# Optimization experiments

Hardware: AMD Instinct MI355X
Metric: run time of the kernel (lower is better)

Reference implementation:

```python
import jax, jax.numpy as jnp
import numpy as np

B, N, F = 2, 512, 64
LN_EPS = 1e-6

def _ln(x, scale, bias):
    mu = jnp.mean(x, axis=-1, keepdims=True)
    var = jnp.mean(jnp.square(x - mu), axis=-1, keepdims=True)
    return (x - mu) * jax.lax.rsqrt(var + LN_EPS) * scale + bias

def setup_inputs() -> dict:
    key = jax.random.key(0)
    k = jax.random.split(key, 16)
    w = lambda kk, s: jax.random.normal(kk, s, jnp.float32) * 0.02
    return {
        'qs': jax.random.normal(k[0], (B, N, F), jnp.float32),
        'ks': jax.random.normal(k[1], (B, N, F), jnp.float32),
        'vs': jax.random.normal(k[2], (B, N, F), jnp.float32),
        'qs_s': jax.random.normal(k[3], (B, N, 2), jnp.float32),
        'ks_s': jax.random.normal(k[4], (B, N, 2), jnp.float32),
        'qs_t': jax.random.uniform(k[5], (B, N, 1), dtype=jnp.float32),
        'ks_t': jax.random.uniform(k[6], (B, N, 1), dtype=jnp.float32),
        'valid_lens': jax.random.randint(k[7], (B,), 1, N + 1),
        'Wv': w(k[8], (F, 64)), 'bv': jnp.zeros((64,), jnp.float32),
        'Wa1': w(k[9], (2 * F + 5, 256)), 'ba1': jnp.zeros((256,), jnp.float32),
        'Wa2': w(k[10], (256, 256)), 'ba2': jnp.zeros((256,), jnp.float32),
        'Wa3': w(k[11], (256, 1)), 'ba3': jnp.zeros((1,), jnp.float32),
        'Wg1': w(k[12], (64, 256)), 'bg1': jnp.zeros((256,), jnp.float32),
        'Wg2': w(k[13], (256, 64)), 'bg2': jnp.zeros((64,), jnp.float32),
        'ln1_s': jnp.ones((64,), jnp.float32), 'ln1_b': jnp.zeros((64,), jnp.float32),
        'ln2_s': jnp.ones((64,), jnp.float32), 'ln2_b': jnp.zeros((64,), jnp.float32),
    }

def reference(qs, ks, vs, qs_s, ks_s, qs_t, ks_t, valid_lens,
              Wv, bv, Wa1, ba1, Wa2, ba2, Wa3, ba3,
              Wg1, bg1, Wg2, bg2, ln1_s, ln1_b, ln2_s, ln2_b):
    Bb, Q, Ff = qs.shape
    K = ks.shape[1]
    # pairwise broadcast-concat features: (B, Q, K, 2F+5)
    qb = jnp.broadcast_to(qs[:, :, None, :], (Bb, Q, K, Ff))
    kb = jnp.broadcast_to(ks[:, None, :, :], (Bb, Q, K, Ff))
    s_diff = qs_s[:, :, None, :] - ks_s[:, None, :, :]            # (B,Q,K,2)
    s_dist = jnp.linalg.norm(s_diff, axis=-1, keepdims=True)      # (B,Q,K,1)
    t_diff = qs_t[:, :, None, :] - ks_t[:, None, :, :]            # (B,Q,K,1)
    m = jnp.concatenate([qb, kb, s_diff, s_dist, jnp.square(s_dist), t_diff], axis=-1)
    # validity mask over the node axis (Q == K node-set attention)
    v_mask = (jnp.arange(K)[None, :] < valid_lens[:, None])[..., None]  # (B,K,1)
    mask = jnp.logical_and(v_mask, t_diff[..., 0] > 0)                   # (B,Q,K)
    # per-pair MLP attention score
    h = jax.nn.gelu(m @ Wa1 + ba1)
    h = jax.nn.gelu(h @ Wa2 + ba2)
    attn = (h @ Wa3 + ba3)[..., 0]                                       # (B,Q,K)
    attn = jnp.where(mask, attn, 0.0)
    vproj = vs @ Wv + bv                                                 # (B,K,64)
    ctx = _ln(jnp.einsum('bqk,bkd->bqd', attn, vproj), ln1_s, ln1_b)     # (B,Q,64)
    gate = jax.nn.gelu(ctx @ Wg1 + bg1) @ Wg2 + bg2                      # (B,Q,64)
    pooled = jnp.max(jnp.where(v_mask, gate * ctx, -jnp.inf), axis=1)    # (B,64)
    vnode = _ln(pooled, ln2_s, ln2_b)
    return ctx, vnode
```

## Files before the change

kernel.cpp:

```cpp
#include <hip/hip_runtime.h>
#include <math.h>

#define BB 2
#define NN 512
#define FF 64
#define HH 256
#define LN_EPS 1e-6f

typedef __attribute__((ext_vector_type(8))) short short8v;
typedef __attribute__((ext_vector_type(4))) float float4v;

#define LDAH 264

#if __has_builtin(__builtin_amdgcn_exp2f)
#define EXP2F(x) __builtin_amdgcn_exp2f(x)
#else
#define EXP2F(x) exp2f(x)
#endif
#if __has_builtin(__builtin_amdgcn_sqrtf)
#define SQRTF(x) __builtin_amdgcn_sqrtf(x)
#else
#define SQRTF(x) sqrtf(x)
#endif

__device__ __forceinline__ float gelu_tanh(float x) {
    float x2 = x * x;
    float t  = __builtin_fmaf(0.10294340f, x2, 2.30211830f);
    float e  = EXP2F(x * t);
    float r  = __builtin_amdgcn_rcpf(e + 1.0f);
    return __builtin_fmaf(-x, r, x);
}

__device__ __forceinline__ unsigned short f2bf(float f) {
    unsigned u = __float_as_uint(f);
    unsigned r = u + 0x7fffu + ((u >> 16) & 1u);
    return (unsigned short)(r >> 16);
}

__device__ __forceinline__ unsigned enc_f(float f) {
    unsigned b = __float_as_uint(f);
    return (b & 0x80000000u) ? ~b : (b | 0x80000000u);
}
__device__ __forceinline__ float dec_f(unsigned u) {
    return __uint_as_float((u & 0x80000000u) ? (u ^ 0x80000000u) : ~u);
}

__global__ __launch_bounds__(256) void prep_kernel(
    const float* __restrict__ qs, const float* __restrict__ ks,
    const float* __restrict__ vs,
    const float* __restrict__ Wa1, const float* __restrict__ ba1,
    const float* __restrict__ Wv,  const float* __restrict__ bv,
    const float* __restrict__ Wa2,
    const float* __restrict__ qs_t, const float* __restrict__ ks_t,
    const int*   __restrict__ valid_lens,
    float* __restrict__ Aq, float* __restrict__ Ak,
    float* __restrict__ vproj, unsigned short* __restrict__ Wa2T,
    int* __restrict__ klist, int* __restrict__ wl_count, int* __restrict__ wl,
    float* __restrict__ ctx_zero) {
    __shared__ int s_cnt[8];
    __shared__ int s_off[9];
    const int bid = blockIdx.x;
    const int t   = threadIdx.x;
    if (bid < 1024) {
        int idx = bid * 256 + t;
        int j  = idx & (HH - 1);
        int bn = idx >> 8;
        const float* qrow = qs + bn * FF;
        const float* krow = ks + bn * FF;
        float aq = ba1[j];
        float ak = 0.0f;
#pragma unroll 8
        for (int f = 0; f < FF; ++f) {
            aq += qrow[f] * Wa1[f * HH + j];
            ak += krow[f] * Wa1[(FF + f) * HH + j];
        }
        Aq[idx] = aq;
        Ak[idx] = ak;
    } else if (bid < 1280) {
        int idx = (bid - 1024) * 256 + t;
        int d  = idx & 63;
        int bn = idx >> 6;
        const float* vrow = vs + bn * FF;
        float a = bv[d];
#pragma unroll 8
        for (int f = 0; f < FF; ++f) a += vrow[f] * Wv[f * 64 + d];
        vproj[idx] = a;
        ctx_zero[idx] = 0.0f;
    } else if (bid < 1536) {
        int idx = (bid - 1280) * 256 + t;
        int n = idx >> 8;
        int i = idx & 255;
        Wa2T[idx] = f2bf(Wa2[i * HH + n]);
    } else {
        const int bq = bid - 1536;
        const int b  = bq >> 9;
        const int q  = bq & 511;
        if (q >= valid_lens[b]) return;
        const float qt = qs_t[bq];
        const int lane = t & 63;
        const int w    = t >> 6;
        bool validr[2];
        int  posr[2];
#pragma unroll
        for (int r = 0; r < 2; ++r) {
            int k = r * 256 + t;
            float kt = ks_t[b * NN + k];
            bool valid = (qt - kt) > 0.0f;
            unsigned long long bal = __ballot(valid);
            validr[r] = valid;
            posr[r] = (int)__popcll(bal & ((1ull << lane) - 1ull));
            if (lane == 0) s_cnt[r * 4 + w] = (int)__popcll(bal);
        }
        __syncthreads();
        if (t == 0) {
            int acc = 0;
#pragma unroll
            for (int i = 0; i < 8; ++i) { s_off[i] = acc; acc += s_cnt[i]; }
            s_off[8] = acc;
        }
        __syncthreads();
#pragma unroll
        for (int r = 0; r < 2; ++r)
            if (validr[r])
                klist[bq * 512 + s_off[r * 4 + w] + posr[r]] = r * 256 + t;
        const int nk = s_off[8];
        if (t == 0 && nk > 0) {
            int nch = (nk + 63) >> 6;
            int base = atomicAdd(wl_count, nch);
            for (int c = 0; c < nch; ++c) {
                int nv = nk - (c << 6);
                nv = nv > 64 ? 64 : nv;
                wl[base + c] = bq | (c << 10) | (nv << 13);
            }
        }
    }
}

__global__ __launch_bounds__(256, 3) void attn_ctx_kernel(
    const float* __restrict__ ks_s, const float* __restrict__ qs_s,
    const float* __restrict__ qs_t, const float* __restrict__ ks_t,
    const float* __restrict__ Wa1,
    const unsigned short* __restrict__ Wa2T,
    const float* __restrict__ ba2, const float* __restrict__ Wa3,
    const float* __restrict__ ba3,
    const float* __restrict__ Aq,  const float* __restrict__ Ak,
    const float* __restrict__ vproj,
    const int* __restrict__ klist, const int* __restrict__ wl_count,
    const int* __restrict__ wl,
    float* __restrict__ ctx_acc_g) {

    __shared__ unsigned short s_h1[64 * LDAH];
    __shared__ float4 s_feat4[64];
    __shared__ int    s_koe[64];
    __shared__ int    s_kvo[64];
    __shared__ float  s_part[4 * 64];
    __shared__ float  s_attn[64];

    const int i = blockIdx.x;
    if (i >= wl_count[0]) return;

    const int t    = threadIdx.x;
    const int lane = t & 63;
    const int w    = t >> 6;
    const int l15  = lane & 15;
    const int quad = lane >> 4;

    const int e  = wl[i];
    const int bq = e & 1023;
    const int c  = (e >> 10) & 7;
    const int nv = (e >> 13) & 127;
    const int b  = bq >> 9;

    const int n0 = w * 64;
    const unsigned short* bbase = Wa2T + (size_t)(n0 + l15) * HH + quad * 8;
    short8v Bcur[4];
#pragma unroll
    for (int nt = 0; nt < 4; ++nt)
        Bcur[nt] = *(const short8v*)(bbase + (size_t)nt * 16 * HH);

    const float qt   = qs_t[bq];
    const float qss0 = qs_s[bq * 2 + 0];
    const float qss1 = qs_s[bq * 2 + 1];
    if (t < 64) {
        int k = klist[bq * 512 + c * 64 + ((t < nv) ? t : 0)];
        int bk = b * NN + k;
        float d0 = qss0 - ks_s[bk * 2 + 0];
        float d1 = qss1 - ks_s[bk * 2 + 1];
        float dist = SQRTF(d0 * d0 + d1 * d1);
        float td = qt - ks_t[bk];
        s_feat4[t] = make_float4(d0, d1, dist, td);
        s_koe[t] = bk * HH;
        s_kvo[t] = bk * 64;
    }
    __syncthreads();

    {
        const int jp = (t & 127) * 2;
        const int kh = (t >> 7) * 32;
        const float2 aqv = *(const float2*)(Aq + bq * HH + jp);
        const float2 w0v = *(const float2*)(Wa1 + 128 * HH + jp);
        const float2 w1v = *(const float2*)(Wa1 + 129 * HH + jp);
        const float2 w2v = *(const float2*)(Wa1 + 130 * HH + jp);
        const float2 w3v = *(const float2*)(Wa1 + 131 * HH + jp);
        const float2 w4v = *(const float2*)(Wa1 + 132 * HH + jp);
        const float* __restrict__ Akj = Ak + jp;
        unsigned* __restrict__ s_h1w = (unsigned*)s_h1;
        const int colw = t & 127;
#pragma unroll
        for (int g = 0; g < 4; ++g) {
            float2 akv[8];
#pragma unroll
            for (int u = 0; u < 8; ++u)
                akv[u] = *(const float2*)(Akj + s_koe[kh + g * 8 + u]);
#pragma unroll
            for (int u = 0; u < 8; ++u) {
                const int kl = kh + g * 8 + u;
                float4 f = s_feat4[kl];
                float fz2 = f.z * f.z;
                float v0 = aqv.x + akv[u].x + w0v.x * f.x + w1v.x * f.y
                         + w2v.x * f.z + w3v.x * fz2 + w4v.x * f.w;
                float v1 = aqv.y + akv[u].y + w0v.y * f.x + w1v.y * f.y
                         + w2v.y * f.z + w3v.y * fz2 + w4v.y * f.w;
                unsigned lo = f2bf(gelu_tanh(v0));
                unsigned hi = f2bf(gelu_tanh(v1));
                s_h1w[kl * (LDAH / 2) + colw] = lo | (hi << 16);
            }
        }
    }
    __syncthreads();

    float4v acc[4][4];
#pragma unroll
    for (int mt = 0; mt < 4; ++mt)
#pragma unroll
        for (int nt = 0; nt < 4; ++nt) acc[mt][nt] = (float4v){0.f, 0.f, 0.f, 0.f};
    const unsigned short* abase = s_h1 + l15 * LDAH + quad * 8;
#pragma unroll
    for (int ksx = 0; ksx < 8; ++ksx) {
        short8v Bnxt[4];
        if (ksx < 7) {
            const int k1 = (ksx + 1) * 32;
#pragma unroll
            for (int nt = 0; nt < 4; ++nt)
                Bnxt[nt] = *(const short8v*)(bbase + (size_t)nt * 16 * HH + k1);
        }
        short8v Af[4];
        const int k0 = ksx * 32;
#pragma unroll
        for (int mt = 0; mt < 4; ++mt)
            Af[mt] = *(const short8v*)(abase + mt * 16 * LDAH + k0);
#pragma unroll
        for (int mt = 0; mt < 4; ++mt)
#pragma unroll
            for (int nt = 0; nt < 4; ++nt)
                acc[mt][nt] = __builtin_amdgcn_mfma_f32_16x16x32_bf16(
                    Af[mt], Bcur[nt], acc[mt][nt], 0, 0, 0);
        if (ksx < 7) {
#pragma unroll
            for (int nt = 0; nt < 4; ++nt) Bcur[nt] = Bnxt[nt];
        }
    }

    {
        float ba2r[4], wa3r[4];
#pragma unroll
        for (int nt = 0; nt < 4; ++nt) {
            int col = n0 + nt * 16 + l15;
            ba2r[nt] = ba2[col];
            wa3r[nt] = Wa3[col];
        }
        float prow[4][4];
#pragma unroll
        for (int mt = 0; mt < 4; ++mt)
#pragma unroll
            for (int r = 0; r < 4; ++r) prow[mt][r] = 0.0f;
#pragma unroll
        for (int mt = 0; mt < 4; ++mt)
#pragma unroll
            for (int nt = 0; nt < 4; ++nt)
#pragma unroll
                for (int r = 0; r < 4; ++r)
                    prow[mt][r] += gelu_tanh(acc[mt][nt][r] + ba2r[nt]) * wa3r[nt];
#pragma unroll
        for (int m = 1; m < 16; m <<= 1)
#pragma unroll
            for (int mt = 0; mt < 4; ++mt)
#pragma unroll
                for (int r = 0; r < 4; ++r)
                    prow[mt][r] += __shfl_xor(prow[mt][r], m);
        if (l15 == 0) {
#pragma unroll
            for (int mt = 0; mt < 4; ++mt)
#pragma unroll
                for (int r = 0; r < 4; ++r)
                    s_part[w * 64 + mt * 16 + quad * 4 + r] = prow[mt][r];
        }
    }
    __syncthreads();

    if (t < 64) {
        float a = 0.0f;
        if (t < nv)
            a = s_part[t] + s_part[64 + t] + s_part[128 + t] + s_part[192 + t] + ba3[0];
        s_attn[t] = a;
    }
    __syncthreads();

    {
        float cacc = 0.0f;
#pragma unroll
        for (int g = 0; g < 2; ++g) {
            float vv[8];
#pragma unroll
            for (int u = 0; u < 8; ++u)
                vv[u] = vproj[s_kvo[w * 16 + g * 8 + u] + lane];
#pragma unroll
            for (int u = 0; u < 8; ++u)
                cacc += s_attn[w * 16 + g * 8 + u] * vv[u];
        }
        s_part[w * 64 + lane] = cacc;
    }
    __syncthreads();
    if (t < 64) {
        float v = s_part[t] + s_part[64 + t] + s_part[128 + t] + s_part[192 + t];
        atomicAdd(&ctx_acc_g[bq * 64 + t], v);
    }
}

__global__ __launch_bounds__(256) void gate_kernel(
    float* __restrict__ ctx,
    const float* __restrict__ ln1_s, const float* __restrict__ ln1_b,
    const float* __restrict__ Wg1, const float* __restrict__ bg1,
    const float* __restrict__ Wg2, const float* __restrict__ bg2,
    const int* __restrict__ valid_lens,
    unsigned* __restrict__ pooled) {
    __shared__ float s_ctx[64];
    __shared__ float s_hg[256];
    const int t  = threadIdx.x;
    const int bq = blockIdx.x;
    const int b  = bq >> 9;
    const int q  = bq & 511;
    if (t < 64) {
        float x = ctx[bq * 64 + t];
        float s = x;
#pragma unroll
        for (int m = 1; m < 64; m <<= 1) s += __shfl_xor(s, m);
        float mu = s * (1.0f / 64.0f);
        float dv = x - mu;
        float vv = dv * dv;
#pragma unroll
        for (int m = 1; m < 64; m <<= 1) vv += __shfl_xor(vv, m);
        float rs = rsqrtf(vv * (1.0f / 64.0f) + LN_EPS);
        float y = dv * rs * ln1_s[t] + ln1_b[t];
        ctx[bq * 64 + t] = y;
        s_ctx[t] = y;
    }
    __syncthreads();
    if (q >= valid_lens[b]) return;
    float a = bg1[t];
#pragma unroll 8
    for (int d = 0; d < 64; ++d) a += s_ctx[d] * Wg1[d * 256 + t];
    s_hg[t] = gelu_tanh(a);
    __syncthreads();
    if (t < 64) {
        float g = bg2[t];
#pragma unroll 8
        for (int jj = 0; jj < 256; ++jj) g += s_hg[jj] * Wg2[jj * 64 + t];
        atomicMax(&pooled[b * 64 + t], enc_f(g * s_ctx[t]));
    }
}

__global__ __launch_bounds__(64) void ln2_kernel(
    const unsigned* __restrict__ pooled,
    const float* __restrict__ ln2_s, const float* __restrict__ ln2_b,
    float* __restrict__ vnode_out) {
    const int t = threadIdx.x;
    const int b = blockIdx.x;
    float x = dec_f(pooled[b * 64 + t]);
    float s = x;
#pragma unroll
    for (int mm = 1; mm < 64; mm <<= 1) s += __shfl_xor(s, mm);
    float mu = s * (1.0f / 64.0f);
    float dv = x - mu;
    float vv = dv * dv;
#pragma unroll
    for (int mm = 1; mm < 64; mm <<= 1) vv += __shfl_xor(vv, mm);
    float rs = rsqrtf(vv * (1.0f / 64.0f) + LN_EPS);
    vnode_out[b * 64 + t] = dv * rs * ln2_s[t] + ln2_b[t];
}

extern "C" void kernel_launch(void* const* d_in, const int* in_sizes, int n_in,
                              void* d_out, int out_size, void* d_ws, size_t ws_size,
                              hipStream_t stream) {
    const float* qs   = (const float*)d_in[0];
    const float* ks   = (const float*)d_in[1];
    const float* vs   = (const float*)d_in[2];
    const float* qs_s = (const float*)d_in[3];
    const float* ks_s = (const float*)d_in[4];
    const float* qs_t = (const float*)d_in[5];
    const float* ks_t = (const float*)d_in[6];
    const int*   valid_lens = (const int*)d_in[7];
    const float* Wv   = (const float*)d_in[8];
    const float* bv   = (const float*)d_in[9];
    const float* Wa1  = (const float*)d_in[10];
    const float* ba1  = (const float*)d_in[11];
    const float* Wa2  = (const float*)d_in[12];
    const float* ba2  = (const float*)d_in[13];
    const float* Wa3  = (const float*)d_in[14];
    const float* ba3  = (const float*)d_in[15];
    const float* Wg1  = (const float*)d_in[16];
    const float* bg1  = (const float*)d_in[17];
    const float* Wg2  = (const float*)d_in[18];
    const float* bg2  = (const float*)d_in[19];
    const float* ln1_s = (const float*)d_in[20];
    const float* ln1_b = (const float*)d_in[21];
    const float* ln2_s = (const float*)d_in[22];
    const float* ln2_b = (const float*)d_in[23];

    float* out = (float*)d_out;
    float* ws  = (float*)d_ws;
    float* Aq    = ws;
    float* Ak    = Aq + BB * NN * HH;
    float* vproj = Ak + BB * NN * HH;
    unsigned short* Wa2T = (unsigned short*)(vproj + BB * NN * 64);
    int* klist = (int*)(Wa2T + HH * HH);
    int* wl_count = klist + BB * NN * 512;
    unsigned* pooled = (unsigned*)(wl_count + 64);
    int* wl = (int*)(pooled + 128);

    hipMemsetAsync(wl_count, 0, 192 * sizeof(int), stream);
    prep_kernel<<<2560, 256, 0, stream>>>(qs, ks, vs, Wa1, ba1, Wv, bv, Wa2,
                                          qs_t, ks_t, valid_lens,
                                          Aq, Ak, vproj, Wa2T, klist, wl_count, wl, out);
    attn_ctx_kernel<<<8192, 256, 0, stream>>>(ks_s, qs_s, qs_t, ks_t,
                                              Wa1, Wa2T, ba2, Wa3, ba3,
                                              Aq, Ak, vproj,
                                              klist, wl_count, wl, out);
    gate_kernel<<<BB * NN, 256, 0, stream>>>(out, ln1_s, ln1_b, Wg1, bg1, Wg2, bg2,
                                             valid_lens, pooled);
    ln2_kernel<<<BB, 64, 0, stream>>>(pooled, ln2_s, ln2_b, out + BB * NN * 64);
}
```

Before: 204.6 us.

## Replace atomic worklist with fixed-slot worklist and drop memset launch

The worklist is now built in fixed slots of eight per query row, so the atomic counter and the hipMemsetAsync launch are no longer needed. Pooled buffer zeroing moves into prep_kernel, and invalid query rows get ctx pre-set to ln1_b so gate_kernel can exit early for them. Empty chunks make attention blocks return immediately, at the cost of losing the compact ordering of work items. The loads of Ak and vproj are also regrouped into wider batches to expose more memory-level parallelism, which raises register pressure.

```diff
diff --git a/kernel.cpp b/kernel.cpp
--- a/kernel.cpp
+++ b/kernel.cpp
@@ -53,10 +53,12 @@
     const float* __restrict__ Wa2,
     const float* __restrict__ qs_t, const float* __restrict__ ks_t,
     const int*   __restrict__ valid_lens,
+    const float* __restrict__ ln1_b,
     float* __restrict__ Aq, float* __restrict__ Ak,
     float* __restrict__ vproj, unsigned short* __restrict__ Wa2T,
-    int* __restrict__ klist, int* __restrict__ wl_count, int* __restrict__ wl,
-    float* __restrict__ ctx_zero) {
+    int* __restrict__ klist, int* __restrict__ wl,
+    unsigned* __restrict__ pooled,
+    float* __restrict__ ctx_init) {
     __shared__ int s_cnt[8];
     __shared__ int s_off[9];
     const int bid = blockIdx.x;
@@ -85,8 +87,11 @@
 #pragma unroll 8
         for (int f = 0; f < FF; ++f) a += vrow[f] * Wv[f * 64 + d];
         vproj[idx] = a;
-        ctx_zero[idx] = 0.0f;
+        int q = bn & 511;
+        int b = bn >> 9;
+        ctx_init[idx] = (q < valid_lens[b]) ? 0.0f : ln1_b[d];
     } else if (bid < 1536) {
+        if (bid == 1280 && t < 128) pooled[t] = 0u;
         int idx = (bid - 1280) * 256 + t;
         int n = idx >> 8;
         int i = idx & 255;
@@ -95,7 +100,10 @@
         const int bq = bid - 1536;
         const int b  = bq >> 9;
         const int q  = bq & 511;
-        if (q >= valid_lens[b]) return;
+        if (q >= valid_lens[b]) {
+            if (t < 8) wl[bq * 8 + t] = bq | (t << 10);
+            return;
+        }
         const float qt = qs_t[bq];
         const int lane = t & 63;
         const int w    = t >> 6;
@@ -124,14 +132,10 @@
             if (validr[r])
                 klist[bq * 512 + s_off[r * 4 + w] + posr[r]] = r * 256 + t;
         const int nk = s_off[8];
-        if (t == 0 && nk > 0) {
-            int nch = (nk + 63) >> 6;
-            int base = atomicAdd(wl_count, nch);
-            for (int c = 0; c < nch; ++c) {
-                int nv = nk - (c << 6);
-                nv = nv > 64 ? 64 : nv;
-                wl[base + c] = bq | (c << 10) | (nv << 13);
-            }
+        if (t < 8) {
+            int nv = nk - (t << 6);
+            nv = nv < 0 ? 0 : (nv > 64 ? 64 : nv);
+            wl[bq * 8 + t] = bq | (t << 10) | (nv << 13);
         }
     }
 }
@@ -145,8 +149,7 @@
     const float* __restrict__ ba3,
     const float* __restrict__ Aq,  const float* __restrict__ Ak,
     const float* __restrict__ vproj,
-    const int* __restrict__ klist, const int* __restrict__ wl_count,
-    const int* __restrict__ wl,
+    const int* __restrict__ klist, const int* __restrict__ wl,
     float* __restrict__ ctx_acc_g) {
 
     __shared__ unsigned short s_h1[64 * LDAH];
@@ -156,20 +159,18 @@
     __shared__ float  s_part[4 * 64];
     __shared__ float  s_attn[64];
 
-    const int i = blockIdx.x;
-    if (i >= wl_count[0]) return;
+    const int e  = wl[blockIdx.x];
+    const int nv = (e >> 13) & 127;
+    if (nv == 0) return;
+    const int bq = e & 1023;
+    const int c  = (e >> 10) & 7;
+    const int b  = bq >> 9;
 
     const int t    = threadIdx.x;
     const int lane = t & 63;
     const int w    = t >> 6;
     const int l15  = lane & 15;
     const int quad = lane >> 4;
-
-    const int e  = wl[i];
-    const int bq = e & 1023;
-    const int c  = (e >> 10) & 7;
-    const int nv = (e >> 13) & 127;
-    const int b  = bq >> 9;
 
     const int n0 = w * 64;
     const unsigned short* bbase = Wa2T + (size_t)(n0 + l15) * HH + quad * 8;
@@ -207,14 +208,14 @@
         unsigned* __restrict__ s_h1w = (unsigned*)s_h1;
         const int colw = t & 127;
 #pragma unroll
-        for (int g = 0; g < 4; ++g) {
-            float2 akv[8];
-#pragma unroll
-            for (int u = 0; u < 8; ++u)
-                akv[u] = *(const float2*)(Akj + s_koe[kh + g * 8 + u]);
-#pragma unroll
-            for (int u = 0; u < 8; ++u) {
-                const int kl = kh + g * 8 + u;
+        for (int g = 0; g < 2; ++g) {
+            float2 akv[16];
+#pragma unroll
+            for (int u = 0; u < 16; ++u)
+                akv[u] = *(const float2*)(Akj + s_koe[kh + g * 16 + u]);
+#pragma unroll
+            for (int u = 0; u < 16; ++u) {
+                const int kl = kh + g * 16 + u;
                 float4 f = s_feat4[kl];
                 float fz2 = f.z * f.z;
                 float v0 = aqv.x + akv[u].x + w0v.x * f.x + w1v.x * f.y
@@ -307,17 +308,14 @@
     __syncthreads();
 
     {
+        float vv[16];
+#pragma unroll
+        for (int u = 0; u < 16; ++u)
+            vv[u] = vproj[s_kvo[w * 16 + u] + lane];
         float cacc = 0.0f;
 #pragma unroll
-        for (int g = 0; g < 2; ++g) {
-            float vv[8];
-#pragma unroll
-            for (int u = 0; u < 8; ++u)
-                vv[u] = vproj[s_kvo[w * 16 + g * 8 + u] + lane];
-#pragma unroll
-            for (int u = 0; u < 8; ++u)
-                cacc += s_attn[w * 16 + g * 8 + u] * vv[u];
-        }
+        for (int u = 0; u < 16; ++u)
+            cacc += s_attn[w * 16 + u] * vv[u];
         s_part[w * 64 + lane] = cacc;
     }
     __syncthreads();
@@ -340,6 +338,7 @@
     const int bq = blockIdx.x;
     const int b  = bq >> 9;
     const int q  = bq & 511;
+    if (q >= valid_lens[b]) return;
     if (t < 64) {
         float x = ctx[bq * 64 + t];
         float s = x;
@@ -356,7 +355,6 @@
         s_ctx[t] = y;
     }
     __syncthreads();
-    if (q >= valid_lens[b]) return;
     float a = bg1[t];
 #pragma unroll 8
     for (int d = 0; d < 64; ++d) a += s_ctx[d] * Wg1[d * 256 + t];
@@ -424,18 +422,16 @@
     float* vproj = Ak + BB * NN * HH;
     unsigned short* Wa2T = (unsigned short*)(vproj + BB * NN * 64);
     int* klist = (int*)(Wa2T + HH * HH);
-    int* wl_count = klist + BB * NN * 512;
-    unsigned* pooled = (unsigned*)(wl_count + 64);
+    unsigned* pooled = (unsigned*)(klist + BB * NN * 512);
     int* wl = (int*)(pooled + 128);
 
-    hipMemsetAsync(wl_count, 0, 192 * sizeof(int), stream);
     prep_kernel<<<2560, 256, 0, stream>>>(qs, ks, vs, Wa1, ba1, Wv, bv, Wa2,
-                                          qs_t, ks_t, valid_lens,
-                                          Aq, Ak, vproj, Wa2T, klist, wl_count, wl, out);
+                                          qs_t, ks_t, valid_lens, ln1_b,
+                                          Aq, Ak, vproj, Wa2T, klist, wl, pooled, out);
     attn_ctx_kernel<<<8192, 256, 0, stream>>>(ks_s, qs_s, qs_t, ks_t,
                                               Wa1, Wa2T, ba2, Wa3, ba3,
                                               Aq, Ak, vproj,
-                                              klist, wl_count, wl, out);
+                                              klist, wl, out);
     gate_kernel<<<BB * NN, 256, 0, stream>>>(out, ln1_s, ln1_b, Wg1, bg1, Wg2, bg2,
                                              valid_lens, pooled);
     ln2_kernel<<<BB, 64, 0, stream>>>(pooled, ln2_s, ln2_b, out + BB * NN * 64);
```

Result: slower. 245.6 us (+20.0%).
